# Optimization experiments

Hardware: AMD Instinct MI355X
Metric: run time of the kernel (lower is better)

The kernel has to match this reference:

```python
import jax, jax.numpy as jnp
import numpy as np

N_NODES = 100000
N_EDGES = 1600000
NUM_GRAPHS = 128
F_IN = 64
HID = 64


def setup_inputs() -> dict:
    key = jax.random.key(0)
    ks = jax.random.split(key, 10)
    x = jax.random.normal(ks[0], (N_NODES, F_IN), dtype=jnp.float32)
    edge_index = jax.random.randint(ks[1], (2, N_EDGES), 0, N_NODES, dtype=jnp.int64)
    batch = jnp.sort(jax.random.randint(ks[2], (N_NODES,), 0, NUM_GRAPHS, dtype=jnp.int64))
    def glorot(k, shape):
        lim = float(np.sqrt(6.0 / (shape[0] + shape[1])))
        return jax.random.uniform(k, shape, dtype=jnp.float32, minval=-lim, maxval=lim)
    return {
        "x": x,
        "edge_index": edge_index,
        "batch": batch,
        "W1": glorot(ks[3], (F_IN, HID)), "b1": jnp.zeros((HID,), jnp.float32),
        "W2": glorot(ks[4], (HID, HID)), "b2": jnp.zeros((HID,), jnp.float32),
        "W3": glorot(ks[5], (HID, HID)), "b3": jnp.zeros((HID,), jnp.float32),
        "fc1_w": glorot(ks[6], (HID, 10)), "fc1_b": jnp.zeros((10,), jnp.float32),
        "fc2_w": glorot(ks[7], (10, 1)), "fc2_b": jnp.zeros((1,), jnp.float32),
    }


def reference(x, edge_index, batch, W1, b1, W2, b2, W3, b3, fc1_w, fc1_b, fc2_w, fc2_b):
    n = x.shape[0]
    # GCN normalization with self-loops (PyG gcn_norm): deg over dst incl. self-loop
    loop = jnp.arange(n, dtype=edge_index.dtype)
    src = jnp.concatenate([edge_index[0], loop])
    dst = jnp.concatenate([edge_index[1], loop])
    deg = jax.ops.segment_sum(jnp.ones_like(dst, dtype=x.dtype), dst, num_segments=n)
    dinv = jnp.where(deg > 0, jax.lax.rsqrt(deg), 0.0)
    norm = (dinv[src] * dinv[dst])[:, None]  # [E+N, 1]

    def gcn_conv(h, W, b):
        h = h @ W                      # dense linear transform
        msg = h[src] * norm            # gather + degree normalize
        agg = jax.ops.segment_sum(msg, dst, num_segments=n)  # scatter-add
        return agg + b

    h = jax.nn.relu(gcn_conv(x, W1, b1))
    h = jax.nn.relu(gcn_conv(h, W2, b2))
    h = jax.nn.relu(gcn_conv(h, W3, b3))

    # global mean pool over graphs
    sums = jax.ops.segment_sum(h, batch, num_segments=NUM_GRAPHS)
    counts = jax.ops.segment_sum(jnp.ones((n,), h.dtype), batch, num_segments=NUM_GRAPHS)
    pooled = sums / jnp.maximum(counts, 1.0)[:, None]  # [NUM_GRAPHS, HID]

    out = jax.nn.relu(pooled @ fc1_w + fc1_b)
    return out @ fc2_w + fc2_b  # [NUM_GRAPHS, 1]
```

## Files before the change

kernel.cpp:

```cpp
#include <hip/hip_runtime.h>
#include <hip/hip_fp16.h>

#define N_NODES   100000
#define N_EDGES   1600000
#define NUM_GRAPHS 128
#define HID       64

#define NB   512
#define NPB  196
#define NBU  511
#define CPE  3125
#define CSR_TOT (N_EDGES + N_NODES)


__global__ void k_f2h(const float* __restrict__ in, __half* __restrict__ out, int n4) {
  int i = blockIdx.x * blockDim.x + threadIdx.x;
  if (i >= n4) return;
  float4 v = ((const float4*)in)[i];
  ((__half2*)out)[2 * i]     = __floats2half2_rn(v.x, v.y);
  ((__half2*)out)[2 * i + 1] = __floats2half2_rn(v.z, v.w);
}

__global__ __launch_bounds__(256) void k_b1a(const int* __restrict__ dst, int* __restrict__ H) {
  __shared__ int hist[NB];
  int w = blockIdx.x, t = threadIdx.x;
  for (int b = t; b < NB; b += 256) hist[b] = 0;
  __syncthreads();
  int e0 = w * CPE;
  for (int i = t; i < CPE; i += 256)
    atomicAdd(&hist[dst[e0 + i] / NPB], 1);
  __syncthreads();
  for (int b = t; b < NB; b += 256) H[w * NB + b] = hist[b];
}

__global__ __launch_bounds__(256) void k_colsum(const int* __restrict__ H, int* __restrict__ S) {
  __shared__ int red[256];
  int b = blockIdx.x, t = threadIdx.x;
  red[t] = H[t * NB + b] + H[(t + 256) * NB + b];
  __syncthreads();
  for (int d = 128; d > 0; d >>= 1) { if (t < d) red[t] += red[t + d]; __syncthreads(); }
  if (t == 0) S[b] = red[0];
}

__global__ __launch_bounds__(512) void k_rowscan(const int* __restrict__ H,
                                                 const int* __restrict__ S,
                                                 int* __restrict__ bstart,
                                                 int* __restrict__ OT,
                                                 int* __restrict__ dbins) {
  __shared__ int sb[NB];
  __shared__ int sc[NB];
  int b = blockIdx.x, t = threadIdx.x;
  if (t < 256) dbins[t] = 0;
  int sv = S[t];
  sb[t] = sv; __syncthreads();
  for (int d = 1; d < NB; d <<= 1) {
    int x = (t >= d) ? sb[t - d] : 0; __syncthreads();
    sb[t] += x; __syncthreads();
  }
  int bst = sb[b] - S[b];
  if (t == 0) bstart[b] = bst;
  if (b == NB - 1 && t == 0) bstart[NB] = sb[NB - 1];
  int v = H[t * NB + b];
  sc[t] = v; __syncthreads();
  for (int d = 1; d < NB; d <<= 1) {
    int x = (t >= d) ? sc[t - d] : 0; __syncthreads();
    sc[t] += x; __syncthreads();
  }
  OT[b * NB + t] = bst + sc[t] - v;
}

__global__ __launch_bounds__(256) void k_b1b(const int* __restrict__ src,
                                             const int* __restrict__ dst,
                                             const int* __restrict__ OT,
                                             int2* __restrict__ staged) {
  __shared__ int pos[NB];
  int w = blockIdx.x, t = threadIdx.x;
  for (int b = t; b < NB; b += 256) pos[b] = OT[b * NB + w];
  __syncthreads();
  int e0 = w * CPE;
  for (int i = t; i < CPE; i += 256) {
    int s = src[e0 + i], d = dst[e0 + i];
    int p = atomicAdd(&pos[d / NPB], 1);
    staged[p] = make_int2(s, d);
  }
}

__global__ __launch_bounds__(256) void k_b2a(const int2* __restrict__ staged,
                                             const int* __restrict__ bstart,
                                             int* __restrict__ row_off,
                                             float* __restrict__ dinv,
                                             int* __restrict__ dbins) {
  __shared__ int cnt[256];
  __shared__ int sc[256];
  __shared__ int hb[256];
  int b = blockIdx.x, t = threadIdx.x;
  int nloc = min(NPB, N_NODES - b * NPB);
  cnt[t] = 0;
  hb[t] = 0;
  __syncthreads();
  int s0 = bstart[b], s1 = bstart[b + 1];
  for (int i = s0 + t; i < s1; i += 256)
    atomicAdd(&cnt[staged[i].y - b * NPB], 1);
  __syncthreads();
  if (t < nloc) atomicAdd(&hb[min(cnt[t] + 1, 255)], 1);
  int v = (t < nloc) ? cnt[t] + 1 : 0;
  sc[t] = v; __syncthreads();
  for (int d = 1; d < 256; d <<= 1) {
    int x = (t >= d) ? sc[t - d] : 0; __syncthreads();
    sc[t] += x; __syncthreads();
  }
  if (t < nloc) {
    int g = b * NPB + t;
    row_off[g] = bstart[b] + b * NPB + (sc[t] - v);
    dinv[g] = rsqrtf((float)(cnt[t] + 1));
  }
  __syncthreads();
  if (hb[t] > 0) atomicAdd(&dbins[t], hb[t]);
  if (b == 0 && t == 0) row_off[N_NODES] = CSR_TOT;
}

__global__ __launch_bounds__(256) void k_b2b(const int2* __restrict__ staged,
                                             const int* __restrict__ bstart,
                                             const int* __restrict__ row_off,
                                             const float* __restrict__ dinv,
                                             int2* __restrict__ csr) {
  __shared__ int pos[NPB];
  __shared__ float dl[NPB];
  int b = blockIdx.x, t = threadIdx.x;
  int nloc = min(NPB, N_NODES - b * NPB);
  if (t < nloc) {
    int g = b * NPB + t;
    int ro = row_off[g];
    float dv = dinv[g];
    csr[ro] = make_int2(g, __float_as_int(dv * dv));
    pos[t] = ro + 1;
    dl[t] = dv;
  }
  __syncthreads();
  int s0 = bstart[b], s1 = bstart[b + 1];
  for (int i = s0 + t; i < s1; i += 256) {
    int2 e = staged[i];
    int l = e.y - b * NPB;
    int p = atomicAdd(&pos[l], 1);
    csr[p] = make_int2(e.x, __float_as_int(dl[l] * dinv[e.x]));
  }
}

__global__ __launch_bounds__(256) void k_dscan(const int* __restrict__ dbins,
                                               int* __restrict__ dpos,
                                               float* __restrict__ pooled,
                                               int* __restrict__ pcnt) {
  __shared__ int sc[256];
  int t = threadIdx.x;
  #pragma unroll
  for (int i = 0; i < 32; ++i) pooled[i * 256 + t] = 0.f;
  if (t < 128) pcnt[t] = 0;
  int v = dbins[t];
  sc[t] = v; __syncthreads();
  for (int d = 1; d < 256; d <<= 1) {
    int x = (t >= d) ? sc[t - d] : 0; __syncthreads();
    sc[t] += x; __syncthreads();
  }
  dpos[t] = sc[t] - v;
}

__global__ __launch_bounds__(256) void k_dperm(const int* __restrict__ row_off,
                                               int* __restrict__ dpos,
                                               int* __restrict__ perm) {
  __shared__ int cnt[256];
  __shared__ int sbase[256];
  int t = threadIdx.x;
  cnt[t] = 0;
  __syncthreads();
  int v = blockIdx.x * 256 + t;
  int bin = 0, rank = 0;
  if (v < N_NODES) {
    bin = min(row_off[v + 1] - row_off[v], 255);
    rank = atomicAdd(&cnt[bin], 1);
  }
  __syncthreads();
  if (cnt[t] > 0) sbase[t] = atomicAdd(&dpos[t], cnt[t]);
  __syncthreads();
  if (v < N_NODES) perm[sbase[bin] + rank] = v;
}


__global__ __launch_bounds__(256) void k_gemm(const __half* __restrict__ A,
                                              const float* __restrict__ W,
                                              __half* __restrict__ C) {
  __shared__ float sW[64 * 64];
  __shared__ float sA[64][65];
  int tid = threadIdx.x;
  #pragma unroll
  for (int i = tid; i < 1024; i += 256)
    ((float4*)sW)[i] = ((const float4*)W)[i];
  int row0 = blockIdx.x * 64;
  #pragma unroll
  for (int i = tid; i < 1024; i += 256) {
    int r = i >> 4, c4 = (i & 15) << 2;
    int row = row0 + r;
    if (row < N_NODES) {
      __half2 a = *(const __half2*)(A + (size_t)row * 64 + c4);
      __half2 b = *(const __half2*)(A + (size_t)row * 64 + c4 + 2);
      float2 fa = __half22float2(a), fb = __half22float2(b);
      sA[r][c4 + 0] = fa.x; sA[r][c4 + 1] = fa.y;
      sA[r][c4 + 2] = fb.x; sA[r][c4 + 3] = fb.y;
    } else {
      sA[r][c4 + 0] = 0.f; sA[r][c4 + 1] = 0.f; sA[r][c4 + 2] = 0.f; sA[r][c4 + 3] = 0.f;
    }
  }
  __syncthreads();
  int tr = (tid >> 4) << 2;
  int tc = (tid & 15) << 2;
  float acc[4][4];
  #pragma unroll
  for (int i = 0; i < 4; ++i)
    #pragma unroll
    for (int j = 0; j < 4; ++j) acc[i][j] = 0.f;
  #pragma unroll 8
  for (int k = 0; k < 64; ++k) {
    float4 w = *(const float4*)&sW[k * 64 + tc];
    float a0 = sA[tr + 0][k], a1 = sA[tr + 1][k], a2 = sA[tr + 2][k], a3 = sA[tr + 3][k];
    acc[0][0] += a0 * w.x; acc[0][1] += a0 * w.y; acc[0][2] += a0 * w.z; acc[0][3] += a0 * w.w;
    acc[1][0] += a1 * w.x; acc[1][1] += a1 * w.y; acc[1][2] += a1 * w.z; acc[1][3] += a1 * w.w;
    acc[2][0] += a2 * w.x; acc[2][1] += a2 * w.y; acc[2][2] += a2 * w.z; acc[2][3] += a2 * w.w;
    acc[3][0] += a3 * w.x; acc[3][1] += a3 * w.y; acc[3][2] += a3 * w.z; acc[3][3] += a3 * w.w;
  }
  #pragma unroll
  for (int i = 0; i < 4; ++i) {
    int row = row0 + tr + i;
    if (row < N_NODES) {
      *(__half2*)(C + (size_t)row * 64 + tc)     = __floats2half2_rn(acc[i][0], acc[i][1]);
      *(__half2*)(C + (size_t)row * 64 + tc + 2) = __floats2half2_rn(acc[i][2], acc[i][3]);
    }
  }
}


__device__ __forceinline__ void fma8(float* acc, float n, uint4 h) {
  __half2 u0 = *(__half2*)&h.x, u1 = *(__half2*)&h.y;
  __half2 u2 = *(__half2*)&h.z, u3 = *(__half2*)&h.w;
  float2 f0 = __half22float2(u0), f1 = __half22float2(u1);
  float2 f2 = __half22float2(u2), f3 = __half22float2(u3);
  acc[0] = fmaf(n, f0.x, acc[0]); acc[1] = fmaf(n, f0.y, acc[1]);
  acc[2] = fmaf(n, f1.x, acc[2]); acc[3] = fmaf(n, f1.y, acc[3]);
  acc[4] = fmaf(n, f2.x, acc[4]); acc[5] = fmaf(n, f2.y, acc[5]);
  acc[6] = fmaf(n, f3.x, acc[6]); acc[7] = fmaf(n, f3.y, acc[7]);
}

__device__ __forceinline__ int2 nt_load_i2(const int2* p) {
  unsigned long long raw = __builtin_nontemporal_load((const unsigned long long*)p);
  int2 r;
  r.x = (int)(unsigned int)(raw & 0xffffffffULL);
  r.y = (int)(unsigned int)(raw >> 32);
  return r;
}

__global__ __launch_bounds__(256) void k_agg(const __half* __restrict__ hw,
                                             const int* __restrict__ row_off,
                                             const int2* __restrict__ csr,
                                             const int* __restrict__ perm,
                                             const float* __restrict__ bias,
                                             __half* __restrict__ out) {
  int tid = threadIdx.x;
  int lane = tid & 63;
  int sg = lane >> 3;
  int k = lane & 7;
  int slot = (blockIdx.x * 4 + (tid >> 6)) * 8 + sg;
  int v = -1, o = 0, d = 1;
  if (slot < N_NODES) {
    v = perm[slot];
    o = row_off[v];
    d = row_off[v + 1] - o;
  }
  int m = d;
  m = max(m, __shfl_xor(m, 8));
  m = max(m, __shfl_xor(m, 16));
  m = max(m, __shfl_xor(m, 32));
  float acc[8];
  #pragma unroll
  for (int j = 0; j < 8; ++j) acc[j] = 0.f;
  const __half* hk = hw + k * 8;
  int dm1 = d - 1;
  int i = 0;
  for (; i + 8 <= m; i += 8) {
    int2 p[8];
    uint4 h[8];
    #pragma unroll
    for (int j = 0; j < 8; ++j) p[j] = nt_load_i2(csr + o + min(i + j, dm1));
    #pragma unroll
    for (int j = 0; j < 8; ++j) h[j] = *(const uint4*)(hk + (size_t)p[j].x * 64);
    #pragma unroll
    for (int j = 0; j < 8; ++j) {
      float n = (i + j < d) ? __int_as_float(p[j].y) : 0.f;
      fma8(acc, n, h[j]);
    }
  }
  for (; i < m; ++i) {
    int2 p = nt_load_i2(csr + o + min(i, dm1));
    uint4 h = *(const uint4*)(hk + (size_t)p.x * 64);
    float n = (i < d) ? __int_as_float(p.y) : 0.f;
    fma8(acc, n, h);
  }
  if (v >= 0) {
    float4 b0 = *(const float4*)(bias + k * 8);
    float4 b1 = *(const float4*)(bias + k * 8 + 4);
    __half2 q0 = __floats2half2_rn(fmaxf(acc[0] + b0.x, 0.f), fmaxf(acc[1] + b0.y, 0.f));
    __half2 q1 = __floats2half2_rn(fmaxf(acc[2] + b0.z, 0.f), fmaxf(acc[3] + b0.w, 0.f));
    __half2 q2 = __floats2half2_rn(fmaxf(acc[4] + b1.x, 0.f), fmaxf(acc[5] + b1.y, 0.f));
    __half2 q3 = __floats2half2_rn(fmaxf(acc[6] + b1.z, 0.f), fmaxf(acc[7] + b1.w, 0.f));
    uint4 r;
    r.x = *(unsigned int*)&q0; r.y = *(unsigned int*)&q1;
    r.z = *(unsigned int*)&q2; r.w = *(unsigned int*)&q3;
    *(uint4*)(out + (size_t)v * HID + k * 8) = r;
  }
}


#define POOL_CHUNK 32

__global__ __launch_bounds__(256) void k_pool(const __half* __restrict__ h,
                                              const int* __restrict__ batch,
                                              float* __restrict__ pooled,
                                              int* __restrict__ pcnt) {
  int wid = threadIdx.x >> 6, lane = threadIdx.x & 63;
  int w = blockIdx.x * (blockDim.x >> 6) + wid;
  int v0 = w * POOL_CHUNK;
  if (v0 >= N_NODES) return;
  int vend = min(v0 + POOL_CHUNK, N_NODES);
  int g = batch[v0];
  float acc = 0.0f;
  int cnt = 0;
  for (int v = v0; v < vend; ++v) {
    int gv = batch[v];
    if (gv != g) {
      atomicAdd(&pooled[g * HID + lane], acc);
      if (lane == 0) atomicAdd(&pcnt[g], cnt);
      g = gv; acc = 0.0f; cnt = 0;
    }
    acc += __half2float(h[(size_t)v * HID + lane]);
    ++cnt;
  }
  atomicAdd(&pooled[g * HID + lane], acc);
  if (lane == 0) atomicAdd(&pcnt[g], cnt);
}

__global__ void k_mlp(const float* __restrict__ pooled, const int* __restrict__ pcnt,
                      const float* __restrict__ fc1w, const float* __restrict__ fc1b,
                      const float* __restrict__ fc2w, const float* __restrict__ fc2b,
                      float* __restrict__ out) {
  int g = threadIdx.x;
  if (g >= NUM_GRAPHS) return;
  float inv = 1.0f / fmaxf((float)pcnt[g], 1.0f);
  float hid[10];
  #pragma unroll
  for (int j = 0; j < 10; ++j) hid[j] = fc1b[j];
  for (int k = 0; k < HID; ++k) {
    float p = pooled[g * HID + k] * inv;
    #pragma unroll
    for (int j = 0; j < 10; ++j) hid[j] += p * fc1w[k * 10 + j];
  }
  float o = fc2b[0];
  #pragma unroll
  for (int j = 0; j < 10; ++j) o += fmaxf(hid[j], 0.0f) * fc2w[j];
  out[g] = o;
}


extern "C" void kernel_launch(void* const* d_in, const int* in_sizes, int n_in,
                              void* d_out, int out_size, void* d_ws, size_t ws_size,
                              hipStream_t stream) {
  const float* x    = (const float*)d_in[0];
  const int*   ei   = (const int*)d_in[1];
  const int*   batch= (const int*)d_in[2];
  const float* W1   = (const float*)d_in[3];
  const float* b1   = (const float*)d_in[4];
  const float* W2   = (const float*)d_in[5];
  const float* b2   = (const float*)d_in[6];
  const float* W3   = (const float*)d_in[7];
  const float* b3   = (const float*)d_in[8];
  const float* fc1w = (const float*)d_in[9];
  const float* fc1b = (const float*)d_in[10];
  const float* fc2w = (const float*)d_in[11];
  const float* fc2b = (const float*)d_in[12];

  const int* e_src = ei;
  const int* e_dst = ei + N_EDGES;

  char* ws = (char*)d_ws;
  auto alignup = [](size_t o, size_t a) { return (o + a - 1) / a * a; };
  size_t off = 0;
  int*   H      = (int*)(ws + off);  off += (size_t)NB * NB * 4;
  int*   pcnt   = (int*)(ws + off);  off += 128 * 4;
  float* pooled = (float*)(ws + off); off += 8192 * 4;
  int*   dbins  = (int*)(ws + off);  off += 256 * 4;
  int*   S      = (int*)(ws + off);  off += NB * 4;
  int*   bstart = (int*)(ws + off);  off += (NB + 1) * 4;
  int*   dpos   = (int*)(ws + off);  off += 256 * 4;       off = alignup(off, 256);
  int*   OT     = (int*)(ws + off);  off += (size_t)NB * NB * 4;          off = alignup(off, 256);
  int*   row_off= (int*)(ws + off);  off += (size_t)(N_NODES + 1) * 4;    off = alignup(off, 256);
  float* dinv   = (float*)(ws + off); off += (size_t)N_NODES * 4;         off = alignup(off, 256);
  int*   perm   = (int*)(ws + off);  off += (size_t)N_NODES * 4;          off = alignup(off, 256);
  int2*  csr    = (int2*)(ws + off); off += (size_t)CSR_TOT * 8;          off = alignup(off, 256);
  __half* xh    = (__half*)(ws + off); off += (size_t)N_NODES * HID * 2;  off = alignup(off, 256);
  __half* h_a   = (__half*)(ws + off); off += (size_t)N_NODES * HID * 2;  off = alignup(off, 256);
  int2*  staged = (int2*)(ws + off);
  __half* h_b   = (__half*)(ws + off); off += (size_t)N_EDGES * 8;
  (void)ws_size; (void)in_sizes; (void)n_in; (void)out_size;

  const int TB = 256;
  const int NGRID = (N_NODES + TB - 1) / TB;
  k_f2h    <<<(N_NODES * HID / 4 + TB - 1) / TB, TB, 0, stream>>>(x, xh, N_NODES * HID / 4);
  k_b1a    <<<NB, TB, 0, stream>>>(e_dst, H);
  k_colsum <<<NB, TB, 0, stream>>>(H, S);
  k_rowscan<<<NB, 512, 0, stream>>>(H, S, bstart, OT, dbins);
  k_b1b    <<<NB, TB, 0, stream>>>(e_src, e_dst, OT, staged);
  k_b2a    <<<NBU, TB, 0, stream>>>(staged, bstart, row_off, dinv, dbins);
  k_b2b    <<<NBU, TB, 0, stream>>>(staged, bstart, row_off, dinv, csr);
  k_dscan  <<<1, TB, 0, stream>>>(dbins, dpos, pooled, pcnt);
  k_dperm  <<<NGRID, TB, 0, stream>>>(row_off, dpos, perm);

  const int GEMM_GRID = (N_NODES + 63) / 64;
  const int AGG_GRID  = (N_NODES + 31) / 32;

  k_gemm<<<GEMM_GRID, TB, 0, stream>>>(xh, W1, h_a);
  k_agg <<<AGG_GRID, TB, 0, stream>>>(h_a, row_off, csr, perm, b1, h_b);
  k_gemm<<<GEMM_GRID, TB, 0, stream>>>(h_b, W2, h_a);
  k_agg <<<AGG_GRID, TB, 0, stream>>>(h_a, row_off, csr, perm, b2, h_b);
  k_gemm<<<GEMM_GRID, TB, 0, stream>>>(h_b, W3, h_a);
  k_agg <<<AGG_GRID, TB, 0, stream>>>(h_a, row_off, csr, perm, b3, h_b);

  const int POOL_GRID = ((N_NODES + POOL_CHUNK - 1) / POOL_CHUNK + 3) / 4;
  k_pool<<<POOL_GRID, TB, 0, stream>>>(h_b, batch, pooled, pcnt);
  k_mlp <<<1, 128, 0, stream>>>(pooled, pcnt, fc1w, fc1b, fc2w, fc2b, (float*)d_out);
}
```

Baseline: 280.6 us.

## Slice node features into 16-wide panels and pack CSR entries into 32 bits

```diff
diff --git a/kernel.cpp b/kernel.cpp
--- a/kernel.cpp
+++ b/kernel.cpp
@@ -12,14 +12,24 @@
 #define CPE  3125
 #define CSR_TOT (N_EDGES + N_NODES)
 
+#define SLICES 4
+#define FPS 16
+#define PASS_BLOCKS ((N_NODES + 63) / 64)
+
+#define SL(p, v, f) (((size_t)(p) * N_NODES + (v)) * FPS + (f))
+
 
 __global__ void k_f2h(const float* __restrict__ in, __half* __restrict__ out, int n4) {
   int i = blockIdx.x * blockDim.x + threadIdx.x;
   if (i >= n4) return;
   float4 v = ((const float4*)in)[i];
-  ((__half2*)out)[2 * i]     = __floats2half2_rn(v.x, v.y);
-  ((__half2*)out)[2 * i + 1] = __floats2half2_rn(v.z, v.w);
-}
+  int row = i >> 4;
+  int c4 = (i & 15) << 2;
+  __half* o = out + SL(c4 >> 4, row, c4 & 15);
+  ((__half2*)o)[0] = __floats2half2_rn(v.x, v.y);
+  ((__half2*)o)[1] = __floats2half2_rn(v.z, v.w);
+}
+
 
 __global__ __launch_bounds__(256) void k_b1a(const int* __restrict__ dst, int* __restrict__ H) {
   __shared__ int hist[NB];
@@ -119,11 +129,16 @@
   if (b == 0 && t == 0) row_off[N_NODES] = CSR_TOT;
 }
 
+__device__ __forceinline__ unsigned int enc_csr(int s, float n) {
+  unsigned short bits = __half_as_ushort(__float2half_rn(n));
+  return ((unsigned int)s << 15) | (unsigned int)(bits & 0x7fff);
+}
+
 __global__ __launch_bounds__(256) void k_b2b(const int2* __restrict__ staged,
                                              const int* __restrict__ bstart,
                                              const int* __restrict__ row_off,
                                              const float* __restrict__ dinv,
-                                             int2* __restrict__ csr) {
+                                             unsigned int* __restrict__ csr4) {
   __shared__ int pos[NPB];
   __shared__ float dl[NPB];
   int b = blockIdx.x, t = threadIdx.x;
@@ -132,7 +147,7 @@
     int g = b * NPB + t;
     int ro = row_off[g];
     float dv = dinv[g];
-    csr[ro] = make_int2(g, __float_as_int(dv * dv));
+    csr4[ro] = enc_csr(g, dv * dv);
     pos[t] = ro + 1;
     dl[t] = dv;
   }
@@ -142,9 +157,10 @@
     int2 e = staged[i];
     int l = e.y - b * NPB;
     int p = atomicAdd(&pos[l], 1);
-    csr[p] = make_int2(e.x, __float_as_int(dl[l] * dinv[e.x]));
-  }
-}
+    csr4[p] = enc_csr(e.x, dl[l] * dinv[e.x]);
+  }
+}
+
 
 __global__ __launch_bounds__(256) void k_dscan(const int* __restrict__ dbins,
                                                int* __restrict__ dpos,
@@ -200,9 +216,9 @@
     int r = i >> 4, c4 = (i & 15) << 2;
     int row = row0 + r;
     if (row < N_NODES) {
-      __half2 a = *(const __half2*)(A + (size_t)row * 64 + c4);
-      __half2 b = *(const __half2*)(A + (size_t)row * 64 + c4 + 2);
-      float2 fa = __half22float2(a), fb = __half22float2(b);
+      const __half* a = A + SL(c4 >> 4, row, c4 & 15);
+      float2 fa = __half22float2(((const __half2*)a)[0]);
+      float2 fb = __half22float2(((const __half2*)a)[1]);
       sA[r][c4 + 0] = fa.x; sA[r][c4 + 1] = fa.y;
       sA[r][c4 + 2] = fb.x; sA[r][c4 + 3] = fb.y;
     } else {
@@ -230,43 +246,44 @@
   for (int i = 0; i < 4; ++i) {
     int row = row0 + tr + i;
     if (row < N_NODES) {
-      *(__half2*)(C + (size_t)row * 64 + tc)     = __floats2half2_rn(acc[i][0], acc[i][1]);
-      *(__half2*)(C + (size_t)row * 64 + tc + 2) = __floats2half2_rn(acc[i][2], acc[i][3]);
+      __half* c = C + SL(tc >> 4, row, tc & 15);
+      ((__half2*)c)[0] = __floats2half2_rn(acc[i][0], acc[i][1]);
+      ((__half2*)c)[1] = __floats2half2_rn(acc[i][2], acc[i][3]);
     }
   }
 }
 
 
-__device__ __forceinline__ void fma8(float* acc, float n, uint4 h) {
-  __half2 u0 = *(__half2*)&h.x, u1 = *(__half2*)&h.y;
-  __half2 u2 = *(__half2*)&h.z, u3 = *(__half2*)&h.w;
-  float2 f0 = __half22float2(u0), f1 = __half22float2(u1);
-  float2 f2 = __half22float2(u2), f3 = __half22float2(u3);
+__device__ __forceinline__ void fma4(float* acc, float n, uint2 h) {
+  float2 f0 = __half22float2(*(__half2*)&h.x);
+  float2 f1 = __half22float2(*(__half2*)&h.y);
   acc[0] = fmaf(n, f0.x, acc[0]); acc[1] = fmaf(n, f0.y, acc[1]);
   acc[2] = fmaf(n, f1.x, acc[2]); acc[3] = fmaf(n, f1.y, acc[3]);
-  acc[4] = fmaf(n, f2.x, acc[4]); acc[5] = fmaf(n, f2.y, acc[5]);
-  acc[6] = fmaf(n, f3.x, acc[6]); acc[7] = fmaf(n, f3.y, acc[7]);
-}
-
-__device__ __forceinline__ int2 nt_load_i2(const int2* p) {
-  unsigned long long raw = __builtin_nontemporal_load((const unsigned long long*)p);
-  int2 r;
-  r.x = (int)(unsigned int)(raw & 0xffffffffULL);
-  r.y = (int)(unsigned int)(raw >> 32);
-  return r;
-}
-
-__global__ __launch_bounds__(256) void k_agg(const __half* __restrict__ hw,
-                                             const int* __restrict__ row_off,
-                                             const int2* __restrict__ csr,
-                                             const int* __restrict__ perm,
-                                             const float* __restrict__ bias,
-                                             __half* __restrict__ out) {
+}
+
+__device__ __forceinline__ unsigned int nt_load_u32(const unsigned int* p) {
+  return __builtin_nontemporal_load(p);
+}
+
+__device__ __forceinline__ float dec_norm(unsigned int e) {
+  return __half2float(__ushort_as_half((unsigned short)(e & 0x7fffu)));
+}
+
+__global__ __launch_bounds__(256) void k_aggs(const __half* __restrict__ hs,
+                                              const int* __restrict__ row_off,
+                                              const unsigned int* __restrict__ csr4,
+                                              const int* __restrict__ perm,
+                                              const float* __restrict__ bias,
+                                              __half* __restrict__ outs) {
+  int bid = blockIdx.x;
+  int pass = (bid & 7) >> 1;
+  int wb = (bid >> 3) * 2 + (bid & 1);
+  if (wb >= PASS_BLOCKS) return;
   int tid = threadIdx.x;
   int lane = tid & 63;
-  int sg = lane >> 3;
-  int k = lane & 7;
-  int slot = (blockIdx.x * 4 + (tid >> 6)) * 8 + sg;
+  int sg = lane >> 2;
+  int k = lane & 3;
+  int slot = (wb * 4 + (tid >> 6)) * 16 + sg;
   int v = -1, o = 0, d = 1;
   if (slot < N_NODES) {
     v = perm[slot];
@@ -274,45 +291,40 @@
     d = row_off[v + 1] - o;
   }
   int m = d;
+  m = max(m, __shfl_xor(m, 4));
   m = max(m, __shfl_xor(m, 8));
   m = max(m, __shfl_xor(m, 16));
   m = max(m, __shfl_xor(m, 32));
-  float acc[8];
-  #pragma unroll
-  for (int j = 0; j < 8; ++j) acc[j] = 0.f;
-  const __half* hk = hw + k * 8;
+  float acc[4] = {0.f, 0.f, 0.f, 0.f};
+  const __half* hp = hs + (size_t)pass * N_NODES * FPS + k * 4;
   int dm1 = d - 1;
   int i = 0;
   for (; i + 8 <= m; i += 8) {
-    int2 p[8];
-    uint4 h[8];
+    unsigned int e[8];
+    uint2 h[8];
     #pragma unroll
-    for (int j = 0; j < 8; ++j) p[j] = nt_load_i2(csr + o + min(i + j, dm1));
+    for (int j = 0; j < 8; ++j) e[j] = nt_load_u32(csr4 + o + min(i + j, dm1));
     #pragma unroll
-    for (int j = 0; j < 8; ++j) h[j] = *(const uint4*)(hk + (size_t)p[j].x * 64);
+    for (int j = 0; j < 8; ++j) h[j] = *(const uint2*)(hp + (size_t)(e[j] >> 15) * FPS);
     #pragma unroll
     for (int j = 0; j < 8; ++j) {
-      float n = (i + j < d) ? __int_as_float(p[j].y) : 0.f;
-      fma8(acc, n, h[j]);
+      float n = (i + j < d) ? dec_norm(e[j]) : 0.f;
+      fma4(acc, n, h[j]);
     }
   }
   for (; i < m; ++i) {
-    int2 p = nt_load_i2(csr + o + min(i, dm1));
-    uint4 h = *(const uint4*)(hk + (size_t)p.x * 64);
-    float n = (i < d) ? __int_as_float(p.y) : 0.f;
-    fma8(acc, n, h);
+    unsigned int e = nt_load_u32(csr4 + o + min(i, dm1));
+    uint2 h = *(const uint2*)(hp + (size_t)(e >> 15) * FPS);
+    float n = (i < d) ? dec_norm(e) : 0.f;
+    fma4(acc, n, h);
   }
   if (v >= 0) {
-    float4 b0 = *(const float4*)(bias + k * 8);
-    float4 b1 = *(const float4*)(bias + k * 8 + 4);
-    __half2 q0 = __floats2half2_rn(fmaxf(acc[0] + b0.x, 0.f), fmaxf(acc[1] + b0.y, 0.f));
-    __half2 q1 = __floats2half2_rn(fmaxf(acc[2] + b0.z, 0.f), fmaxf(acc[3] + b0.w, 0.f));
-    __half2 q2 = __floats2half2_rn(fmaxf(acc[4] + b1.x, 0.f), fmaxf(acc[5] + b1.y, 0.f));
-    __half2 q3 = __floats2half2_rn(fmaxf(acc[6] + b1.z, 0.f), fmaxf(acc[7] + b1.w, 0.f));
-    uint4 r;
-    r.x = *(unsigned int*)&q0; r.y = *(unsigned int*)&q1;
-    r.z = *(unsigned int*)&q2; r.w = *(unsigned int*)&q3;
-    *(uint4*)(out + (size_t)v * HID + k * 8) = r;
+    float4 b = *(const float4*)(bias + pass * FPS + k * 4);
+    __half2 q0 = __floats2half2_rn(fmaxf(acc[0] + b.x, 0.f), fmaxf(acc[1] + b.y, 0.f));
+    __half2 q1 = __floats2half2_rn(fmaxf(acc[2] + b.z, 0.f), fmaxf(acc[3] + b.w, 0.f));
+    unsigned long long r = ((unsigned long long)*(unsigned int*)&q1 << 32) |
+                           (unsigned long long)*(unsigned int*)&q0;
+    __builtin_nontemporal_store(r, (unsigned long long*)(outs + SL(pass, v, k * 4)));
   }
 }
 
@@ -328,6 +340,7 @@
   int v0 = w * POOL_CHUNK;
   if (v0 >= N_NODES) return;
   int vend = min(v0 + POOL_CHUNK, N_NODES);
+  int p = lane >> 4, f = lane & 15;
   int g = batch[v0];
   float acc = 0.0f;
   int cnt = 0;
@@ -338,7 +351,7 @@
       if (lane == 0) atomicAdd(&pcnt[g], cnt);
       g = gv; acc = 0.0f; cnt = 0;
     }
-    acc += __half2float(h[(size_t)v * HID + lane]);
+    acc += __half2float(h[SL(p, v, f)]);
     ++cnt;
   }
   atomicAdd(&pooled[g * HID + lane], acc);
@@ -401,7 +414,7 @@
   int*   row_off= (int*)(ws + off);  off += (size_t)(N_NODES + 1) * 4;    off = alignup(off, 256);
   float* dinv   = (float*)(ws + off); off += (size_t)N_NODES * 4;         off = alignup(off, 256);
   int*   perm   = (int*)(ws + off);  off += (size_t)N_NODES * 4;          off = alignup(off, 256);
-  int2*  csr    = (int2*)(ws + off); off += (size_t)CSR_TOT * 8;          off = alignup(off, 256);
+  unsigned int* csr4 = (unsigned int*)(ws + off); off += (size_t)CSR_TOT * 4; off = alignup(off, 256);
   __half* xh    = (__half*)(ws + off); off += (size_t)N_NODES * HID * 2;  off = alignup(off, 256);
   __half* h_a   = (__half*)(ws + off); off += (size_t)N_NODES * HID * 2;  off = alignup(off, 256);
   int2*  staged = (int2*)(ws + off);
@@ -416,19 +429,19 @@
   k_rowscan<<<NB, 512, 0, stream>>>(H, S, bstart, OT, dbins);
   k_b1b    <<<NB, TB, 0, stream>>>(e_src, e_dst, OT, staged);
   k_b2a    <<<NBU, TB, 0, stream>>>(staged, bstart, row_off, dinv, dbins);
-  k_b2b    <<<NBU, TB, 0, stream>>>(staged, bstart, row_off, dinv, csr);
+  k_b2b    <<<NBU, TB, 0, stream>>>(staged, bstart, row_off, dinv, csr4);
   k_dscan  <<<1, TB, 0, stream>>>(dbins, dpos, pooled, pcnt);
   k_dperm  <<<NGRID, TB, 0, stream>>>(row_off, dpos, perm);
 
   const int GEMM_GRID = (N_NODES + 63) / 64;
-  const int AGG_GRID  = (N_NODES + 31) / 32;
+  const int AGGS_GRID = 8 * ((PASS_BLOCKS + 1) / 2);
 
   k_gemm<<<GEMM_GRID, TB, 0, stream>>>(xh, W1, h_a);
-  k_agg <<<AGG_GRID, TB, 0, stream>>>(h_a, row_off, csr, perm, b1, h_b);
+  k_aggs<<<AGGS_GRID, TB, 0, stream>>>(h_a, row_off, csr4, perm, b1, h_b);
   k_gemm<<<GEMM_GRID, TB, 0, stream>>>(h_b, W2, h_a);
-  k_agg <<<AGG_GRID, TB, 0, stream>>>(h_a, row_off, csr, perm, b2, h_b);
+  k_aggs<<<AGGS_GRID, TB, 0, stream>>>(h_a, row_off, csr4, perm, b2, h_b);
   k_gemm<<<GEMM_GRID, TB, 0, stream>>>(h_b, W3, h_a);
-  k_agg <<<AGG_GRID, TB, 0, stream>>>(h_a, row_off, csr, perm, b3, h_b);
+  k_aggs<<<AGGS_GRID, TB, 0, stream>>>(h_a, row_off, csr4, perm, b3, h_b);
 
   const int POOL_GRID = ((N_NODES + POOL_CHUNK - 1) / POOL_CHUNK + 3) / 4;
   k_pool<<<POOL_GRID, TB, 0, stream>>>(h_b, batch, pooled, pcnt);
```

Result: slower. 538.1 us (+91.8%).

## Pack CSR entries into 32 bits and process high-degree nodes first

Applied to the files above, without the earlier changes.

```diff
diff --git a/kernel.cpp b/kernel.cpp
--- a/kernel.cpp
+++ b/kernel.cpp
@@ -20,6 +20,7 @@
   ((__half2*)out)[2 * i]     = __floats2half2_rn(v.x, v.y);
   ((__half2*)out)[2 * i + 1] = __floats2half2_rn(v.z, v.w);
 }
+
 
 __global__ __launch_bounds__(256) void k_b1a(const int* __restrict__ dst, int* __restrict__ H) {
   __shared__ int hist[NB];
@@ -102,7 +103,7 @@
   for (int i = s0 + t; i < s1; i += 256)
     atomicAdd(&cnt[staged[i].y - b * NPB], 1);
   __syncthreads();
-  if (t < nloc) atomicAdd(&hb[min(cnt[t] + 1, 255)], 1);
+  if (t < nloc) atomicAdd(&hb[255 - min(cnt[t] + 1, 255)], 1);
   int v = (t < nloc) ? cnt[t] + 1 : 0;
   sc[t] = v; __syncthreads();
   for (int d = 1; d < 256; d <<= 1) {
@@ -119,11 +120,16 @@
   if (b == 0 && t == 0) row_off[N_NODES] = CSR_TOT;
 }
 
+__device__ __forceinline__ unsigned int enc_csr(int s, float n) {
+  unsigned short bits = __half_as_ushort(__float2half_rn(n));
+  return ((unsigned int)s << 15) | (unsigned int)(bits & 0x7fff);
+}
+
 __global__ __launch_bounds__(256) void k_b2b(const int2* __restrict__ staged,
                                              const int* __restrict__ bstart,
                                              const int* __restrict__ row_off,
                                              const float* __restrict__ dinv,
-                                             int2* __restrict__ csr) {
+                                             unsigned int* __restrict__ csr4) {
   __shared__ int pos[NPB];
   __shared__ float dl[NPB];
   int b = blockIdx.x, t = threadIdx.x;
@@ -132,7 +138,7 @@
     int g = b * NPB + t;
     int ro = row_off[g];
     float dv = dinv[g];
-    csr[ro] = make_int2(g, __float_as_int(dv * dv));
+    csr4[ro] = enc_csr(g, dv * dv);
     pos[t] = ro + 1;
     dl[t] = dv;
   }
@@ -142,9 +148,10 @@
     int2 e = staged[i];
     int l = e.y - b * NPB;
     int p = atomicAdd(&pos[l], 1);
-    csr[p] = make_int2(e.x, __float_as_int(dl[l] * dinv[e.x]));
-  }
-}
+    csr4[p] = enc_csr(e.x, dl[l] * dinv[e.x]);
+  }
+}
+
 
 __global__ __launch_bounds__(256) void k_dscan(const int* __restrict__ dbins,
                                                int* __restrict__ dpos,
@@ -175,7 +182,7 @@
   int v = blockIdx.x * 256 + t;
   int bin = 0, rank = 0;
   if (v < N_NODES) {
-    bin = min(row_off[v + 1] - row_off[v], 255);
+    bin = 255 - min(row_off[v + 1] - row_off[v], 255);
     rank = atomicAdd(&cnt[bin], 1);
   }
   __syncthreads();
@@ -248,17 +255,13 @@
   acc[6] = fmaf(n, f3.x, acc[6]); acc[7] = fmaf(n, f3.y, acc[7]);
 }
 
-__device__ __forceinline__ int2 nt_load_i2(const int2* p) {
-  unsigned long long raw = __builtin_nontemporal_load((const unsigned long long*)p);
-  int2 r;
-  r.x = (int)(unsigned int)(raw & 0xffffffffULL);
-  r.y = (int)(unsigned int)(raw >> 32);
-  return r;
+__device__ __forceinline__ float dec_norm(unsigned int e) {
+  return __half2float(__ushort_as_half((unsigned short)(e & 0x7fffu)));
 }
 
 __global__ __launch_bounds__(256) void k_agg(const __half* __restrict__ hw,
                                              const int* __restrict__ row_off,
-                                             const int2* __restrict__ csr,
+                                             const unsigned int* __restrict__ csr4,
                                              const int* __restrict__ perm,
                                              const float* __restrict__ bias,
                                              __half* __restrict__ out) {
@@ -284,22 +287,23 @@
   int dm1 = d - 1;
   int i = 0;
   for (; i + 8 <= m; i += 8) {
-    int2 p[8];
+    unsigned int e[8];
     uint4 h[8];
     #pragma unroll
-    for (int j = 0; j < 8; ++j) p[j] = nt_load_i2(csr + o + min(i + j, dm1));
+    for (int j = 0; j < 8; ++j)
+      e[j] = __builtin_nontemporal_load(csr4 + o + min(i + j, dm1));
     #pragma unroll
-    for (int j = 0; j < 8; ++j) h[j] = *(const uint4*)(hk + (size_t)p[j].x * 64);
+    for (int j = 0; j < 8; ++j) h[j] = *(const uint4*)(hk + (size_t)(e[j] >> 15) * 64);
     #pragma unroll
     for (int j = 0; j < 8; ++j) {
-      float n = (i + j < d) ? __int_as_float(p[j].y) : 0.f;
+      float n = (i + j < d) ? dec_norm(e[j]) : 0.f;
       fma8(acc, n, h[j]);
     }
   }
   for (; i < m; ++i) {
-    int2 p = nt_load_i2(csr + o + min(i, dm1));
-    uint4 h = *(const uint4*)(hk + (size_t)p.x * 64);
-    float n = (i < d) ? __int_as_float(p.y) : 0.f;
+    unsigned int e = __builtin_nontemporal_load(csr4 + o + min(i, dm1));
+    uint4 h = *(const uint4*)(hk + (size_t)(e >> 15) * 64);
+    float n = (i < d) ? dec_norm(e) : 0.f;
     fma8(acc, n, h);
   }
   if (v >= 0) {
@@ -401,7 +405,7 @@
   int*   row_off= (int*)(ws + off);  off += (size_t)(N_NODES + 1) * 4;    off = alignup(off, 256);
   float* dinv   = (float*)(ws + off); off += (size_t)N_NODES * 4;         off = alignup(off, 256);
   int*   perm   = (int*)(ws + off);  off += (size_t)N_NODES * 4;          off = alignup(off, 256);
-  int2*  csr    = (int2*)(ws + off); off += (size_t)CSR_TOT * 8;          off = alignup(off, 256);
+  unsigned int* csr4 = (unsigned int*)(ws + off); off += (size_t)CSR_TOT * 4; off = alignup(off, 256);
   __half* xh    = (__half*)(ws + off); off += (size_t)N_NODES * HID * 2;  off = alignup(off, 256);
   __half* h_a   = (__half*)(ws + off); off += (size_t)N_NODES * HID * 2;  off = alignup(off, 256);
   int2*  staged = (int2*)(ws + off);
@@ -416,7 +420,7 @@
   k_rowscan<<<NB, 512, 0, stream>>>(H, S, bstart, OT, dbins);
   k_b1b    <<<NB, TB, 0, stream>>>(e_src, e_dst, OT, staged);
   k_b2a    <<<NBU, TB, 0, stream>>>(staged, bstart, row_off, dinv, dbins);
-  k_b2b    <<<NBU, TB, 0, stream>>>(staged, bstart, row_off, dinv, csr);
+  k_b2b    <<<NBU, TB, 0, stream>>>(staged, bstart, row_off, dinv, csr4);
   k_dscan  <<<1, TB, 0, stream>>>(dbins, dpos, pooled, pcnt);
   k_dperm  <<<NGRID, TB, 0, stream>>>(row_off, dpos, perm);
 
@@ -424,11 +428,11 @@
   const int AGG_GRID  = (N_NODES + 31) / 32;
 
   k_gemm<<<GEMM_GRID, TB, 0, stream>>>(xh, W1, h_a);
-  k_agg <<<AGG_GRID, TB, 0, stream>>>(h_a, row_off, csr, perm, b1, h_b);
+  k_agg <<<AGG_GRID, TB, 0, stream>>>(h_a, row_off, csr4, perm, b1, h_b);
   k_gemm<<<GEMM_GRID, TB, 0, stream>>>(h_b, W2, h_a);
-  k_agg <<<AGG_GRID, TB, 0, stream>>>(h_a, row_off, csr, perm, b2, h_b);
+  k_agg <<<AGG_GRID, TB, 0, stream>>>(h_a, row_off, csr4, perm, b2, h_b);
   k_gemm<<<GEMM_GRID, TB, 0, stream>>>(h_b, W3, h_a);
-  k_agg <<<AGG_GRID, TB, 0, stream>>>(h_a, row_off, csr, perm, b3, h_b);
+  k_agg <<<AGG_GRID, TB, 0, stream>>>(h_a, row_off, csr4, perm, b3, h_b);
 
   const int POOL_GRID = ((N_NODES + POOL_CHUNK - 1) / POOL_CHUNK + 3) / 4;
   k_pool<<<POOL_GRID, TB, 0, stream>>>(h_b, batch, pooled, pcnt);
```

New measurement: 288.3 us. +2.7%, slower.
